# Optimization experiments

Hardware: AMD Instinct MI355X
Metric: run time of the kernel (lower is better)

The kernel has to match this reference:

```python
import jax, jax.numpy as jnp
import numpy as np

B, S, E = 4, 2048, 1024

def setup_inputs() -> dict:
    key = jax.random.key(0)
    ks = jax.random.split(key, 7)
    s = 1.0 / np.sqrt(E)
    return {
        "x":  jax.random.normal(ks[0], (B, S, E), jnp.float32),
        "Wq": jax.random.normal(ks[1], (E, E), jnp.float32) * s,
        "bq": jax.random.normal(ks[2], (E,), jnp.float32) * s,
        "Wk": jax.random.normal(ks[3], (E, E), jnp.float32) * s,
        "bk": jax.random.normal(ks[4], (E,), jnp.float32) * s,
        "Wv": jax.random.normal(ks[5], (E, E), jnp.float32) * s,
        "bv": jax.random.normal(ks[6], (E,), jnp.float32) * s,
    }

def reference(x, Wq, bq, Wk, bk, Wv, bv):
    # Linear layers: y = x @ W^T + b (torch nn.Linear convention)
    q = jnp.einsum('bse,fe->bsf', x, Wq) + bq
    k = jnp.einsum('bse,fe->bsf', x, Wk) + bk
    v = jnp.einsum('bse,fe->bsf', x, Wv) + bv
    inv_scale = jnp.asarray(E ** 0.5, x.dtype)
    scores = jnp.einsum('bqe,bke->bqk', q, k) / inv_scale  # [B,S,S]
    attn = jax.nn.softmax(scores, axis=-1)
    # dropout is identity in eval mode (deterministic reference)
    out = jnp.einsum('bqk,bke->bqe', attn, v)
    return out
```

## Files before the change

kernel.cpp:

```cpp
#include <hip/hip_runtime.h>
#include <hip/hip_bf16.h>
#include <cstdint>


typedef __attribute__((ext_vector_type(8))) short bf16x8;
typedef __attribute__((ext_vector_type(4))) float f32x4;

__device__ __forceinline__ unsigned short f2bf(float f) {
  union { float f; uint32_t u; } x; x.f = f;
  uint32_t u = x.u;
  return (unsigned short)((u + 0x7fffu + ((u >> 16) & 1u)) >> 16);
}

__device__ __forceinline__ void async_copy16(const void* g, void* l) {
  __builtin_amdgcn_global_load_lds(
      (const __attribute__((address_space(1))) void*)g,
      (__attribute__((address_space(3))) void*)l, 16, 0, 0);
}

__global__ __launch_bounds__(256) void convert_all(
    const float* __restrict__ x, const float* __restrict__ Wq,
    const float* __restrict__ Wk, const float* __restrict__ Wv,
    unsigned short* __restrict__ xb, unsigned short* __restrict__ Wb,
    float* __restrict__ rowsum) {
  const long X4 = (long)8192 * 1024 / 4;
  const long W4 = (long)1024 * 1024 / 4;
  if (blockIdx.x == gridDim.x - 1) {
    float4* r = (float4*)rowsum;
#pragma unroll
    for (int t = 0; t < 8; ++t)
      r[threadIdx.x + t * 256] = float4{0.f, 0.f, 0.f, 0.f};
    return;
  }
  long i = (long)blockIdx.x * 256 + threadIdx.x;
  const float* src; unsigned short* dst; long off;
  if (i < X4)             { src = x;  dst = xb;                    off = i; }
  else if (i < X4 + W4)   { src = Wq; dst = Wb;                    off = i - X4; }
  else if (i < X4 + 2*W4) { src = Wk; dst = Wb + (long)1024*1024;  off = i - X4 - W4; }
  else                    { src = Wv; dst = Wb + (long)2048*1024;  off = i - X4 - 2*W4; }
  const float4 v = ((const float4*)src)[off];
  ushort4 o;
  o.x = f2bf(v.x); o.y = f2bf(v.y); o.z = f2bf(v.z); o.w = f2bf(v.w);
  ((ushort4*)dst)[off] = o;
}

template <int MODE>
__global__ __launch_bounds__(256, 4) void gemm_bt(
    const unsigned short* __restrict__ Ab, const unsigned short* __restrict__ Bb,
    unsigned short* __restrict__ Cb, float* __restrict__ Cf,
    unsigned short* __restrict__ VT,
    const float* __restrict__ bias0, const float* __restrict__ bias1,
    const float* __restrict__ bias2, float* __restrict__ rowsum,
    int K, int N, float scale, long sA, long sB, long sC) {
  __shared__ unsigned short As[128 * 64];
  __shared__ unsigned short Bs[128 * 64];

  const int z = blockIdx.z;
  const unsigned short* A  = Ab + (long)z * sA;
  const unsigned short* Bm = Bb + (long)z * sB;

  const int tid  = threadIdx.x;
  const int lane = tid & 63;
  const int wave = tid >> 6;
  const int l15  = lane & 15;
  const int quad = lane >> 4;
  const int wm = (wave >> 1) * 64;
  const int wn = (wave & 1) * 64;

  const int bxd  = gridDim.x;
  const int flat = blockIdx.y * bxd + blockIdx.x;
  const int st = flat >> 6;
  const int inside = flat & 63;
  const int nstx = bxd >> 3;
  const int stx = st % nstx;
  const int sty = st / nstx;
  const int tile_m = (stx * 8 + (inside & 7)) * 128;
  const int tile_n = (sty * 8 + (inside >> 3)) * 128;

  const int rs8 = lane >> 3;
  const int kc  = (lane & 7) ^ rs8;
  const long lK = (long)K;
  const unsigned short* gA0 = A  + (long)(tile_m + wave * 32 + rs8) * lK + kc * 8;
  const unsigned short* gB0 = Bm + (long)(tile_n + wave * 32 + rs8) * lK + kc * 8;
  unsigned short* lA = &As[(wave * 32) * 64];
  unsigned short* lB = &Bs[(wave * 32) * 64];

  const int g0 = (0 * 4 + quad) ^ (l15 & 7);
  const int g1 = (1 * 4 + quad) ^ (l15 & 7);

  f32x4 acc[4][4] = {};

  for (int k0 = 0; k0 < K; k0 += 64) {
    __syncthreads();
#pragma unroll
    for (int t = 0; t < 4; ++t) {
      async_copy16(gA0 + (long)t * 8 * lK + k0, lA + t * 8 * 64);
      async_copy16(gB0 + (long)t * 8 * lK + k0, lB + t * 8 * 64);
    }
    __syncthreads();

#pragma unroll
    for (int s = 0; s < 2; ++s) {
      const int gs = s ? g1 : g0;
      bf16x8 af[4], bfr[4];
#pragma unroll
      for (int i = 0; i < 4; ++i)
        af[i] = *(const bf16x8*)&As[(wm + i * 16 + l15) * 64 + gs * 8];
#pragma unroll
      for (int j = 0; j < 4; ++j)
        bfr[j] = *(const bf16x8*)&Bs[(wn + j * 16 + l15) * 64 + gs * 8];
#pragma unroll
      for (int i = 0; i < 4; ++i)
#pragma unroll
        for (int j = 0; j < 4; ++j)
          acc[i][j] = __builtin_amdgcn_mfma_f32_16x16x32_bf16(af[i], bfr[j], acc[i][j], 0, 0, 0);
    }
  }

  if (MODE == 0) {
    const float* bias = (z == 0) ? bias0 : (z == 1) ? bias1 : bias2;
    if (z == 2) {
#pragma unroll
      for (int j = 0; j < 4; ++j) {
        const int col = tile_n + wn + j * 16 + l15;
        const float bv = bias[col];
#pragma unroll
        for (int i = 0; i < 4; ++i) {
          const int row0 = tile_m + wm + i * 16 + quad * 4;
          const int b = row0 >> 11;
          const int sx = row0 & 2047;
          ushort4 o;
          o.x = f2bf(acc[i][j][0] + bv);
          o.y = f2bf(acc[i][j][1] + bv);
          o.z = f2bf(acc[i][j][2] + bv);
          o.w = f2bf(acc[i][j][3] + bv);
          *(ushort4*)&VT[(long)b * 1024 * 2048 + (long)col * 2048 + sx] = o;
        }
      }
    } else {
      unsigned short* Cbz = Cb + (long)z * sC;
#pragma unroll
      for (int j = 0; j < 4; ++j) {
        const int col = tile_n + wn + j * 16 + l15;
        const float bv = bias[col];
#pragma unroll
        for (int i = 0; i < 4; ++i) {
          const int row0 = tile_m + wm + i * 16 + quad * 4;
#pragma unroll
          for (int r = 0; r < 4; ++r)
            Cbz[(long)(row0 + r) * N + col] = f2bf(acc[i][j][r] + bv);
        }
      }
    }
  } else if (MODE == 1) {
    unsigned short* Cbz = Cb + (long)z * sC;
    float part[16];
#pragma unroll
    for (int t = 0; t < 16; ++t) part[t] = 0.0f;
#pragma unroll
    for (int j = 0; j < 4; ++j) {
      const int col = tile_n + wn + j * 16 + l15;
#pragma unroll
      for (int i = 0; i < 4; ++i) {
        const int row0 = tile_m + wm + i * 16 + quad * 4;
#pragma unroll
        for (int r = 0; r < 4; ++r) {
          const float e = __expf(acc[i][j][r] * scale);
          part[i * 4 + r] += e;
          Cbz[(long)(row0 + r) * N + col] = f2bf(e);
        }
      }
    }
#pragma unroll
    for (int t = 0; t < 16; ++t)
#pragma unroll
      for (int o = 1; o < 16; o <<= 1)
        part[t] += __shfl_xor(part[t], o);
    if (l15 == 0) {
#pragma unroll
      for (int i = 0; i < 4; ++i) {
        const int row0 = tile_m + wm + i * 16 + quad * 4;
#pragma unroll
        for (int r = 0; r < 4; ++r)
          atomicAdd(&rowsum[z * 2048 + row0 + r], part[i * 4 + r]);
      }
    }
  } else {
    float* Cfz = Cf + (long)z * sC;
    float inv[16];
#pragma unroll
    for (int i = 0; i < 4; ++i) {
      const int row0 = tile_m + wm + i * 16 + quad * 4;
#pragma unroll
      for (int r = 0; r < 4; ++r)
        inv[i * 4 + r] = 1.0f / rowsum[z * 2048 + row0 + r];
    }
#pragma unroll
    for (int j = 0; j < 4; ++j) {
      const int col = tile_n + wn + j * 16 + l15;
#pragma unroll
      for (int i = 0; i < 4; ++i) {
        const int row0 = tile_m + wm + i * 16 + quad * 4;
#pragma unroll
        for (int r = 0; r < 4; ++r)
          Cfz[(long)(row0 + r) * N + col] = acc[i][j][r] * inv[i * 4 + r];
      }
    }
  }
}

extern "C" void kernel_launch(void* const* d_in, const int* in_sizes, int n_in,
                              void* d_out, int out_size, void* d_ws, size_t ws_size,
                              hipStream_t stream) {
  const float* x  = (const float*)d_in[0];
  const float* Wq = (const float*)d_in[1];
  const float* bq = (const float*)d_in[2];
  const float* Wk = (const float*)d_in[3];
  const float* bk = (const float*)d_in[4];
  const float* Wv = (const float*)d_in[5];
  const float* bv = (const float*)d_in[6];
  float* out = (float*)d_out;

  constexpr int Bt = 4, S = 2048, E = 1024;
  constexpr int M = Bt * S;

  unsigned short* xb = (unsigned short*)d_ws;
  unsigned short* Wb = xb + (size_t)M * E;
  unsigned short* Q  = Wb + (size_t)3 * E * E;
  unsigned short* Kb = Q + (size_t)M * E;
  unsigned short* VT = Kb + (size_t)M * E;
  unsigned short* P  = VT + (size_t)M * E;
  float* rowsum = (float*)(P + (size_t)Bt * S * S);

  const int conv_blocks = (M * E / 4 + 3 * (E * E / 4)) / 256 + 1;
  convert_all<<<dim3(conv_blocks), dim3(256), 0, stream>>>(x, Wq, Wk, Wv, xb, Wb, rowsum);

  gemm_bt<0><<<dim3(M / 128, E / 128, 3), dim3(256), 0, stream>>>(
      xb, Wb, Q, nullptr, VT, bq, bk, bv, nullptr, E, E, 1.0f,
      0L, (long)E * E, (long)M * E);

  gemm_bt<1><<<dim3(S / 128, S / 128, Bt), dim3(256), 0, stream>>>(
      Q, Kb, P, nullptr, nullptr, nullptr, nullptr, nullptr, rowsum,
      E, S, 1.0f / 32.0f, (long)S * E, (long)S * E, (long)S * S);

  gemm_bt<2><<<dim3(S / 128, E / 128, Bt), dim3(256), 0, stream>>>(
      P, VT, nullptr, out, nullptr, nullptr, nullptr, nullptr, rowsum,
      S, E, 1.0f, (long)S * S, (long)E * S, (long)S * E);
}
```

Measured before the change: 236.0 us.

## Double-buffer GEMM LDS with 8-wave larger tiles and XCD-aware block remap

The GEMM kernel moves to 512-thread workgroups with templated larger tiles (up to 256x256) and two LDS buffers. The next K-tile is prefetched with async global-to-LDS loads while the current one is consumed, using explicit vmcnt waits and barriers plus s_setprio around the MFMA bursts. Block indices are remapped across the 8 XCDs instead of using the old 8x8 supertile swizzle. This aims to hide load latency and raise arithmetic intensity, at the cost of more LDS and registers per block and lower occupancy.

```diff
diff --git a/kernel.cpp b/kernel.cpp
--- a/kernel.cpp
+++ b/kernel.cpp
@@ -1,5 +1,4 @@
 #include <hip/hip_runtime.h>
-#include <hip/hip_bf16.h>
 #include <cstdint>
 
 
@@ -16,6 +15,21 @@
   __builtin_amdgcn_global_load_lds(
       (const __attribute__((address_space(1))) void*)g,
       (__attribute__((address_space(3))) void*)l, 16, 0, 0);
+}
+
+#define FENCE() asm volatile("" ::: "memory")
+
+__device__ __forceinline__ void wg_bar() {
+  FENCE();
+  __builtin_amdgcn_s_barrier();
+  FENCE();
+}
+
+template <int N>
+__device__ __forceinline__ void vm_wait() {
+  if constexpr (N == 0)      asm volatile("s_waitcnt vmcnt(0)" ::: "memory");
+  else if constexpr (N == 6) asm volatile("s_waitcnt vmcnt(6)" ::: "memory");
+  else                       asm volatile("s_waitcnt vmcnt(8)" ::: "memory");
 }
 
 __global__ __launch_bounds__(256) void convert_all(
@@ -44,18 +58,38 @@
   ((ushort4*)dst)[off] = o;
 }
 
-template <int MODE>
-__global__ __launch_bounds__(256, 4) void gemm_bt(
+template <int MODE, int BM, int BN, int WM, int WN>
+__global__ __launch_bounds__(512, 2) void gemm_bt(
     const unsigned short* __restrict__ Ab, const unsigned short* __restrict__ Bb,
     unsigned short* __restrict__ Cb, float* __restrict__ Cf,
     unsigned short* __restrict__ VT,
     const float* __restrict__ bias0, const float* __restrict__ bias1,
     const float* __restrict__ bias2, float* __restrict__ rowsum,
     int K, int N, float scale, long sA, long sB, long sC) {
-  __shared__ unsigned short As[128 * 64];
-  __shared__ unsigned short Bs[128 * 64];
-
-  const int z = blockIdx.z;
+  static_assert(WM * WN == 8, "8 waves");
+  static_assert(BN / WN == 64, "per-wave col span must be 64");
+  constexpr int M_rep = BM / WM / 16;
+  constexpr int N_rep = 4;
+  constexpr int PH    = M_rep / 2;
+  constexpr int LA    = BM / 64;
+  constexpr int LB    = BN / 64;
+  constexpr int LOADS = LA + LB;
+
+  __shared__ unsigned short As[2][BM * 64];
+  __shared__ unsigned short Bs[2][BN * 64];
+
+  const int gx = gridDim.x, gy = gridDim.y;
+  const int nwg = gx * gy * (int)gridDim.z;
+  int flat = ((int)blockIdx.z * gy + (int)blockIdx.y) * gx + (int)blockIdx.x;
+  flat = (flat & 7) * (nwg >> 3) + (flat >> 3);
+  const int bx = flat % gx;
+  const int r2 = flat / gx;
+  const int by = r2 % gy;
+  const int z  = r2 / gy;
+
+  const int tile_m = bx * BM;
+  const int tile_n = by * BN;
+
   const unsigned short* A  = Ab + (long)z * sA;
   const unsigned short* Bm = Bb + (long)z * sB;
 
@@ -64,69 +98,94 @@
   const int wave = tid >> 6;
   const int l15  = lane & 15;
   const int quad = lane >> 4;
-  const int wm = (wave >> 1) * 64;
-  const int wn = (wave & 1) * 64;
-
-  const int bxd  = gridDim.x;
-  const int flat = blockIdx.y * bxd + blockIdx.x;
-  const int st = flat >> 6;
-  const int inside = flat & 63;
-  const int nstx = bxd >> 3;
-  const int stx = st % nstx;
-  const int sty = st / nstx;
-  const int tile_m = (stx * 8 + (inside & 7)) * 128;
-  const int tile_n = (sty * 8 + (inside >> 3)) * 128;
+  const int wn   = wave % WN;
+  const int wm   = wave / WN;
+  const int wmr  = wm * (BM / WM);
+  const int wnc  = wn * 64;
 
   const int rs8 = lane >> 3;
   const int kc  = (lane & 7) ^ rs8;
   const long lK = (long)K;
-  const unsigned short* gA0 = A  + (long)(tile_m + wave * 32 + rs8) * lK + kc * 8;
-  const unsigned short* gB0 = Bm + (long)(tile_n + wave * 32 + rs8) * lK + kc * 8;
-  unsigned short* lA = &As[(wave * 32) * 64];
-  unsigned short* lB = &Bs[(wave * 32) * 64];
-
-  const int g0 = (0 * 4 + quad) ^ (l15 & 7);
-  const int g1 = (1 * 4 + quad) ^ (l15 & 7);
-
-  f32x4 acc[4][4] = {};
-
-  for (int k0 = 0; k0 < K; k0 += 64) {
-    __syncthreads();
-#pragma unroll
-    for (int t = 0; t < 4; ++t) {
-      async_copy16(gA0 + (long)t * 8 * lK + k0, lA + t * 8 * 64);
-      async_copy16(gB0 + (long)t * 8 * lK + k0, lB + t * 8 * 64);
-    }
-    __syncthreads();
-
-#pragma unroll
-    for (int s = 0; s < 2; ++s) {
-      const int gs = s ? g1 : g0;
-      bf16x8 af[4], bfr[4];
-#pragma unroll
-      for (int i = 0; i < 4; ++i)
-        af[i] = *(const bf16x8*)&As[(wm + i * 16 + l15) * 64 + gs * 8];
-#pragma unroll
-      for (int j = 0; j < 4; ++j)
-        bfr[j] = *(const bf16x8*)&Bs[(wn + j * 16 + l15) * 64 + gs * 8];
-#pragma unroll
-      for (int i = 0; i < 4; ++i)
-#pragma unroll
-        for (int j = 0; j < 4; ++j)
-          acc[i][j] = __builtin_amdgcn_mfma_f32_16x16x32_bf16(af[i], bfr[j], acc[i][j], 0, 0, 0);
-    }
+  const unsigned short* gA0 = A  + (long)(tile_m + wave * (BM / 8) + rs8) * lK + kc * 8;
+  const unsigned short* gB0 = Bm + (long)(tile_n + wave * (BN / 8) + rs8) * lK + kc * 8;
+
+  auto stage = [&](int k0, int pb) {
+    unsigned short* la = &As[pb][(wave * (BM / 8)) * 64];
+    unsigned short* lb = &Bs[pb][(wave * (BN / 8)) * 64];
+#pragma unroll
+    for (int t = 0; t < LA; ++t)
+      async_copy16(gA0 + (long)(t * 8) * lK + k0, la + t * 8 * 64);
+#pragma unroll
+    for (int t = 0; t < LB; ++t)
+      async_copy16(gB0 + (long)(t * 8) * lK + k0, lb + t * 8 * 64);
+  };
+
+  const int NT = K >> 6;
+  f32x4 acc[M_rep][N_rep] = {};
+
+  stage(0, 0);
+  stage(64, 1);
+  vm_wait<LOADS>();
+  wg_bar();
+
+  int p = 0;
+  for (int t = 0; t < NT; ++t) {
+    const unsigned short* as = &As[p][0];
+    const unsigned short* bs = &Bs[p][0];
+    bf16x8 bfr[N_rep][2];
+#pragma unroll
+    for (int ph = 0; ph < PH; ++ph) {
+      bf16x8 af[2][2];
+#pragma unroll
+      for (int ii = 0; ii < 2; ++ii) {
+        const int row = wmr + (ph * 2 + ii) * 16 + l15;
+#pragma unroll
+        for (int kk = 0; kk < 2; ++kk)
+          af[ii][kk] = *(const bf16x8*)&as[row * 64 + (((kk * 4 + quad) ^ (l15 & 7)) << 3)];
+      }
+      if (ph == 0) {
+#pragma unroll
+        for (int j = 0; j < N_rep; ++j) {
+          const int row = wnc + j * 16 + l15;
+#pragma unroll
+          for (int kk = 0; kk < 2; ++kk)
+            bfr[j][kk] = *(const bf16x8*)&bs[row * 64 + (((kk * 4 + quad) ^ (l15 & 7)) << 3)];
+        }
+      }
+      wg_bar();
+      __builtin_amdgcn_s_setprio(1);
+#pragma unroll
+      for (int ii = 0; ii < 2; ++ii)
+#pragma unroll
+        for (int j = 0; j < N_rep; ++j)
+#pragma unroll
+          for (int kk = 0; kk < 2; ++kk)
+            acc[ph * 2 + ii][j] = __builtin_amdgcn_mfma_f32_16x16x32_bf16(
+                af[ii][kk], bfr[j][kk], acc[ph * 2 + ii][j], 0, 0, 0);
+      __builtin_amdgcn_s_setprio(0);
+      wg_bar();
+    }
+    if (t + 2 < NT) {
+      stage((t + 2) << 6, p);
+      vm_wait<LOADS>();
+      wg_bar();
+    } else if (t + 1 < NT) {
+      vm_wait<0>();
+      wg_bar();
+    }
+    p ^= 1;
   }
 
-  if (MODE == 0) {
+  if constexpr (MODE == 0) {
     const float* bias = (z == 0) ? bias0 : (z == 1) ? bias1 : bias2;
     if (z == 2) {
 #pragma unroll
-      for (int j = 0; j < 4; ++j) {
-        const int col = tile_n + wn + j * 16 + l15;
+      for (int j = 0; j < N_rep; ++j) {
+        const int col = tile_n + wnc + j * 16 + l15;
         const float bv = bias[col];
 #pragma unroll
-        for (int i = 0; i < 4; ++i) {
-          const int row0 = tile_m + wm + i * 16 + quad * 4;
+        for (int i = 0; i < M_rep; ++i) {
+          const int row0 = tile_m + wmr + i * 16 + quad * 4;
           const int b = row0 >> 11;
           const int sx = row0 & 2047;
           ushort4 o;
@@ -140,29 +199,29 @@
     } else {
       unsigned short* Cbz = Cb + (long)z * sC;
 #pragma unroll
-      for (int j = 0; j < 4; ++j) {
-        const int col = tile_n + wn + j * 16 + l15;
+      for (int j = 0; j < N_rep; ++j) {
+        const int col = tile_n + wnc + j * 16 + l15;
         const float bv = bias[col];
 #pragma unroll
-        for (int i = 0; i < 4; ++i) {
-          const int row0 = tile_m + wm + i * 16 + quad * 4;
+        for (int i = 0; i < M_rep; ++i) {
+          const int row0 = tile_m + wmr + i * 16 + quad * 4;
 #pragma unroll
           for (int r = 0; r < 4; ++r)
             Cbz[(long)(row0 + r) * N + col] = f2bf(acc[i][j][r] + bv);
         }
       }
     }
-  } else if (MODE == 1) {
+  } else if constexpr (MODE == 1) {
     unsigned short* Cbz = Cb + (long)z * sC;
-    float part[16];
-#pragma unroll
-    for (int t = 0; t < 16; ++t) part[t] = 0.0f;
-#pragma unroll
-    for (int j = 0; j < 4; ++j) {
-      const int col = tile_n + wn + j * 16 + l15;
-#pragma unroll
-      for (int i = 0; i < 4; ++i) {
-        const int row0 = tile_m + wm + i * 16 + quad * 4;
+    float part[M_rep * 4];
+#pragma unroll
+    for (int t = 0; t < M_rep * 4; ++t) part[t] = 0.0f;
+#pragma unroll
+    for (int j = 0; j < N_rep; ++j) {
+      const int col = tile_n + wnc + j * 16 + l15;
+#pragma unroll
+      for (int i = 0; i < M_rep; ++i) {
+        const int row0 = tile_m + wmr + i * 16 + quad * 4;
 #pragma unroll
         for (int r = 0; r < 4; ++r) {
           const float e = __expf(acc[i][j][r] * scale);
@@ -172,14 +231,14 @@
       }
     }
 #pragma unroll
-    for (int t = 0; t < 16; ++t)
+    for (int t = 0; t < M_rep * 4; ++t)
 #pragma unroll
       for (int o = 1; o < 16; o <<= 1)
         part[t] += __shfl_xor(part[t], o);
     if (l15 == 0) {
 #pragma unroll
-      for (int i = 0; i < 4; ++i) {
-        const int row0 = tile_m + wm + i * 16 + quad * 4;
+      for (int i = 0; i < M_rep; ++i) {
+        const int row0 = tile_m + wmr + i * 16 + quad * 4;
 #pragma unroll
         for (int r = 0; r < 4; ++r)
           atomicAdd(&rowsum[z * 2048 + row0 + r], part[i * 4 + r]);
@@ -187,20 +246,20 @@
     }
   } else {
     float* Cfz = Cf + (long)z * sC;
-    float inv[16];
-#pragma unroll
-    for (int i = 0; i < 4; ++i) {
-      const int row0 = tile_m + wm + i * 16 + quad * 4;
+    float inv[M_rep * 4];
+#pragma unroll
+    for (int i = 0; i < M_rep; ++i) {
+      const int row0 = tile_m + wmr + i * 16 + quad * 4;
 #pragma unroll
       for (int r = 0; r < 4; ++r)
         inv[i * 4 + r] = 1.0f / rowsum[z * 2048 + row0 + r];
     }
 #pragma unroll
-    for (int j = 0; j < 4; ++j) {
-      const int col = tile_n + wn + j * 16 + l15;
-#pragma unroll
-      for (int i = 0; i < 4; ++i) {
-        const int row0 = tile_m + wm + i * 16 + quad * 4;
+    for (int j = 0; j < N_rep; ++j) {
+      const int col = tile_n + wnc + j * 16 + l15;
+#pragma unroll
+      for (int i = 0; i < M_rep; ++i) {
+        const int row0 = tile_m + wmr + i * 16 + quad * 4;
 #pragma unroll
         for (int r = 0; r < 4; ++r)
           Cfz[(long)(row0 + r) * N + col] = acc[i][j][r] * inv[i * 4 + r];
@@ -235,15 +294,15 @@
   const int conv_blocks = (M * E / 4 + 3 * (E * E / 4)) / 256 + 1;
   convert_all<<<dim3(conv_blocks), dim3(256), 0, stream>>>(x, Wq, Wk, Wv, xb, Wb, rowsum);
 
-  gemm_bt<0><<<dim3(M / 128, E / 128, 3), dim3(256), 0, stream>>>(
+  gemm_bt<0, 128, 256, 2, 4><<<dim3(M / 128, E / 256, 3), dim3(512), 0, stream>>>(
       xb, Wb, Q, nullptr, VT, bq, bk, bv, nullptr, E, E, 1.0f,
       0L, (long)E * E, (long)M * E);
 
-  gemm_bt<1><<<dim3(S / 128, S / 128, Bt), dim3(256), 0, stream>>>(
+  gemm_bt<1, 256, 256, 2, 4><<<dim3(S / 256, S / 256, Bt), dim3(512), 0, stream>>>(
       Q, Kb, P, nullptr, nullptr, nullptr, nullptr, nullptr, rowsum,
       E, S, 1.0f / 32.0f, (long)S * E, (long)S * E, (long)S * S);
 
-  gemm_bt<2><<<dim3(S / 128, E / 128, Bt), dim3(256), 0, stream>>>(
+  gemm_bt<2, 256, 128, 4, 2><<<dim3(S / 256, E / 128, Bt), dim3(512), 0, stream>>>(
       P, VT, nullptr, out, nullptr, nullptr, nullptr, nullptr, rowsum,
       S, E, 1.0f, (long)S * S, (long)E * S, (long)S * E);
 }
```

Result: slower. 291.2 us (+23.4%).

## Replace QK^T scores GEMM with 256x256 double-buffered 8-wave pipelined kernel

Applied to the files above, without the earlier changes.

Replaces the generic 128x128 gemm_bt MODE 1 launch for the Q·K^T scores with a dedicated kernel that uses 256x256 tiles, 512 threads and double-buffered LDS. Global-to-LDS async loads for later k-steps are interleaved with MFMA phases, using explicit vmcnt waits, raw barriers and s_setprio. The goal is to hide load latency and raise data reuse per tile, at the cost of much more LDS (128 KB per block) and register pressure, which lowers occupancy. The exp, bf16 store and atomic row-sum epilogue is kept.

```diff
diff --git a/kernel.cpp b/kernel.cpp
--- a/kernel.cpp
+++ b/kernel.cpp
@@ -1,5 +1,4 @@
 #include <hip/hip_runtime.h>
-#include <hip/hip_bf16.h>
 #include <cstdint>
 
 
@@ -16,6 +15,21 @@
   __builtin_amdgcn_global_load_lds(
       (const __attribute__((address_space(1))) void*)g,
       (__attribute__((address_space(3))) void*)l, 16, 0, 0);
+}
+
+#define FENCE() asm volatile("" ::: "memory")
+
+__device__ __forceinline__ void wg_bar() {
+  FENCE();
+  __builtin_amdgcn_s_barrier();
+  FENCE();
+}
+
+template <int N>
+__device__ __forceinline__ void vm_wait() {
+  if constexpr (N == 0)      asm volatile("s_waitcnt vmcnt(0)" ::: "memory");
+  else if constexpr (N == 4) asm volatile("s_waitcnt vmcnt(4)" ::: "memory");
+  else                       asm volatile("s_waitcnt vmcnt(8)" ::: "memory");
 }
 
 __global__ __launch_bounds__(256) void convert_all(
@@ -117,7 +131,7 @@
     }
   }
 
-  if (MODE == 0) {
+  if constexpr (MODE == 0) {
     const float* bias = (z == 0) ? bias0 : (z == 1) ? bias1 : bias2;
     if (z == 2) {
 #pragma unroll
@@ -152,39 +166,6 @@
         }
       }
     }
-  } else if (MODE == 1) {
-    unsigned short* Cbz = Cb + (long)z * sC;
-    float part[16];
-#pragma unroll
-    for (int t = 0; t < 16; ++t) part[t] = 0.0f;
-#pragma unroll
-    for (int j = 0; j < 4; ++j) {
-      const int col = tile_n + wn + j * 16 + l15;
-#pragma unroll
-      for (int i = 0; i < 4; ++i) {
-        const int row0 = tile_m + wm + i * 16 + quad * 4;
-#pragma unroll
-        for (int r = 0; r < 4; ++r) {
-          const float e = __expf(acc[i][j][r] * scale);
-          part[i * 4 + r] += e;
-          Cbz[(long)(row0 + r) * N + col] = f2bf(e);
-        }
-      }
-    }
-#pragma unroll
-    for (int t = 0; t < 16; ++t)
-#pragma unroll
-      for (int o = 1; o < 16; o <<= 1)
-        part[t] += __shfl_xor(part[t], o);
-    if (l15 == 0) {
-#pragma unroll
-      for (int i = 0; i < 4; ++i) {
-        const int row0 = tile_m + wm + i * 16 + quad * 4;
-#pragma unroll
-        for (int r = 0; r < 4; ++r)
-          atomicAdd(&rowsum[z * 2048 + row0 + r], part[i * 4 + r]);
-      }
-    }
   } else {
     float* Cfz = Cf + (long)z * sC;
     float inv[16];
@@ -205,6 +186,132 @@
         for (int r = 0; r < 4; ++r)
           Cfz[(long)(row0 + r) * N + col] = acc[i][j][r] * inv[i * 4 + r];
       }
+    }
+  }
+}
+
+__global__ __launch_bounds__(512, 2) void scores_8ph(
+    const unsigned short* __restrict__ Qb, const unsigned short* __restrict__ Kb,
+    unsigned short* __restrict__ P, float* __restrict__ rowsum) {
+  constexpr int NT = 16;
+  constexpr long SE = 2048L * 1024;
+  constexpr float SC = 1.0f / 32.0f;
+
+  __shared__ unsigned short As[2][2][128 * 64];
+  __shared__ unsigned short Bs[2][2][128 * 64];
+
+  const int z = blockIdx.z;
+  const unsigned short* A  = Qb + (long)z * SE;
+  const unsigned short* Bm = Kb + (long)z * SE;
+  const int tile_m = blockIdx.x * 256;
+  const int tile_n = blockIdx.y * 256;
+
+  const int tid  = threadIdx.x;
+  const int lane = tid & 63;
+  const int wave = tid >> 6;
+  const int l15  = lane & 15;
+  const int quad = lane >> 4;
+
+  const int rs8 = lane >> 3;
+  const int kc  = (lane & 7) ^ rs8;
+  const unsigned short* gA0 = A  + (long)(tile_m + wave * 16 + rs8) * 1024 + kc * 8;
+  const unsigned short* gB0 = Bm + (long)(tile_n + wave * 16 + rs8) * 1024 + kc * 8;
+
+  auto stA = [&](int T, int h) {
+    if (T < NT) {
+      const int pb = T & 1, k0 = T << 6;
+      async_copy16(gA0 + (long)(h * 128) * 1024 + k0,     &As[pb][h][(wave * 16) * 64]);
+      async_copy16(gA0 + (long)(h * 128 + 8) * 1024 + k0, &As[pb][h][(wave * 16 + 8) * 64]);
+    }
+  };
+  auto stB = [&](int T, int h) {
+    if (T < NT) {
+      const int pb = T & 1, k0 = T << 6;
+      async_copy16(gB0 + (long)(h * 128) * 1024 + k0,     &Bs[pb][h][(wave * 16) * 64]);
+      async_copy16(gB0 + (long)(h * 128 + 8) * 1024 + k0, &Bs[pb][h][(wave * 16 + 8) * 64]);
+    }
+  };
+
+  stA(0, 0); stB(0, 0); stB(0, 1); stA(0, 1);
+  stA(1, 0); stB(1, 0);
+  vm_wait<4>();
+  wg_bar();
+
+  f32x4 acc[16][2] = {};
+
+  for (int t = 0; t < NT; ++t) {
+    const int c = t & 1;
+    bf16x8 bfr[2][2];
+#pragma unroll
+    for (int p = 0; p < 4; ++p) {
+      if (p == 0)      stB(t + 1, 1);
+      else if (p == 1) stA(t + 1, 1);
+      else if (p == 2) stA(t + 2, 0);
+      else             stB(t + 2, 0);
+      bf16x8 af[4][2];
+#pragma unroll
+      for (int ii = 0; ii < 4; ++ii) {
+        const int f = p * 4 + ii;
+        const int rih = (f & 7) * 16 + l15;
+#pragma unroll
+        for (int kk = 0; kk < 2; ++kk)
+          af[ii][kk] = *(const bf16x8*)
+              &As[c][f >> 3][rih * 64 + (((kk * 4 + quad) ^ (l15 & 7)) << 3)];
+      }
+      if (p == 0) {
+#pragma unroll
+        for (int j = 0; j < 2; ++j) {
+          const int rih = (wave & 3) * 32 + j * 16 + l15;
+#pragma unroll
+          for (int kk = 0; kk < 2; ++kk)
+            bfr[j][kk] = *(const bf16x8*)
+                &Bs[c][wave >> 2][rih * 64 + (((kk * 4 + quad) ^ (l15 & 7)) << 3)];
+        }
+      }
+      wg_bar();
+      asm volatile("s_waitcnt lgkmcnt(0)" ::: "memory");
+      __builtin_amdgcn_s_setprio(1);
+#pragma unroll
+      for (int ii = 0; ii < 4; ++ii)
+#pragma unroll
+        for (int j = 0; j < 2; ++j)
+#pragma unroll
+          for (int kk = 0; kk < 2; ++kk)
+            acc[p * 4 + ii][j] = __builtin_amdgcn_mfma_f32_16x16x32_bf16(
+                af[ii][kk], bfr[j][kk], acc[p * 4 + ii][j], 0, 0, 0);
+      __builtin_amdgcn_s_setprio(0);
+      if (p == 3) {
+        if (t + 2 < NT)      vm_wait<4>();
+        else if (t + 1 < NT) vm_wait<0>();
+      }
+      wg_bar();
+    }
+  }
+
+  unsigned short* Pz = P + (long)z * (2048L * 2048);
+#pragma unroll
+  for (int f = 0; f < 16; ++f) {
+    float pr[4] = {0.f, 0.f, 0.f, 0.f};
+    const int row0 = tile_m + f * 16 + quad * 4;
+#pragma unroll
+    for (int j = 0; j < 2; ++j) {
+      const int col = tile_n + wave * 32 + j * 16 + l15;
+#pragma unroll
+      for (int r = 0; r < 4; ++r) {
+        const float e = __expf(acc[f][j][r] * SC);
+        pr[r] += e;
+        Pz[(long)(row0 + r) * 2048 + col] = f2bf(e);
+      }
+    }
+#pragma unroll
+    for (int r = 0; r < 4; ++r)
+#pragma unroll
+      for (int o = 1; o < 16; o <<= 1)
+        pr[r] += __shfl_xor(pr[r], o);
+    if (l15 == 0) {
+#pragma unroll
+      for (int r = 0; r < 4; ++r)
+        atomicAdd(&rowsum[z * 2048 + row0 + r], pr[r]);
     }
   }
 }
@@ -239,9 +346,8 @@
       xb, Wb, Q, nullptr, VT, bq, bk, bv, nullptr, E, E, 1.0f,
       0L, (long)E * E, (long)M * E);
 
-  gemm_bt<1><<<dim3(S / 128, S / 128, Bt), dim3(256), 0, stream>>>(
-      Q, Kb, P, nullptr, nullptr, nullptr, nullptr, nullptr, rowsum,
-      E, S, 1.0f / 32.0f, (long)S * E, (long)S * E, (long)S * S);
+  scores_8ph<<<dim3(S / 256, S / 256, Bt), dim3(512), 0, stream>>>(
+      Q, Kb, P, rowsum);
 
   gemm_bt<2><<<dim3(S / 128, E / 128, Bt), dim3(256), 0, stream>>>(
       P, VT, nullptr, out, nullptr, nullptr, nullptr, nullptr, rowsum,
```

Result: slower. 263.1 us (+11.5%).

## Double-buffer LDS tiles with async prefetch in attention GEMMs

Applied to the files above, without the earlier changes.

Adds a double-buffered shared-memory variant of the GEMM kernel. While the current K-tile is being computed, the next tile is fetched with global_load_lds, ordered by explicit vmcnt waits and raw barriers. The aim is to hide global-load latency behind MFMA work in the QK^T and PV GEMMs. The projection GEMM keeps the single-buffer path. LDS use doubles to 64KB per block, which may limit occupancy from the requested 4 blocks per CU.

```diff
diff --git a/kernel.cpp b/kernel.cpp
--- a/kernel.cpp
+++ b/kernel.cpp
@@ -1,5 +1,4 @@
 #include <hip/hip_runtime.h>
-#include <hip/hip_bf16.h>
 #include <cstdint>
 
 
@@ -16,6 +15,21 @@
   __builtin_amdgcn_global_load_lds(
       (const __attribute__((address_space(1))) void*)g,
       (__attribute__((address_space(3))) void*)l, 16, 0, 0);
+}
+
+#define FENCE() asm volatile("" ::: "memory")
+
+__device__ __forceinline__ void wg_bar() {
+  FENCE();
+  __builtin_amdgcn_s_barrier();
+  FENCE();
+}
+
+template <int N>
+__device__ __forceinline__ void vm_wait() {
+  if constexpr (N == 0)      asm volatile("s_waitcnt vmcnt(0)" ::: "memory");
+  else if constexpr (N == 8) asm volatile("s_waitcnt vmcnt(8)" ::: "memory");
+  else                       asm volatile("s_waitcnt vmcnt(4)" ::: "memory");
 }
 
 __global__ __launch_bounds__(256) void convert_all(
@@ -44,7 +58,7 @@
   ((ushort4*)dst)[off] = o;
 }
 
-template <int MODE>
+template <int MODE, int DBUF>
 __global__ __launch_bounds__(256, 4) void gemm_bt(
     const unsigned short* __restrict__ Ab, const unsigned short* __restrict__ Bb,
     unsigned short* __restrict__ Cb, float* __restrict__ Cf,
@@ -52,8 +66,9 @@
     const float* __restrict__ bias0, const float* __restrict__ bias1,
     const float* __restrict__ bias2, float* __restrict__ rowsum,
     int K, int N, float scale, long sA, long sB, long sC) {
-  __shared__ unsigned short As[128 * 64];
-  __shared__ unsigned short Bs[128 * 64];
+  constexpr int NBUF = DBUF ? 2 : 1;
+  __shared__ unsigned short As[NBUF][128 * 64];
+  __shared__ unsigned short Bs[NBUF][128 * 64];
 
   const int z = blockIdx.z;
   const unsigned short* A  = Ab + (long)z * sA;
@@ -82,42 +97,68 @@
   const long lK = (long)K;
   const unsigned short* gA0 = A  + (long)(tile_m + wave * 32 + rs8) * lK + kc * 8;
   const unsigned short* gB0 = Bm + (long)(tile_n + wave * 32 + rs8) * lK + kc * 8;
-  unsigned short* lA = &As[(wave * 32) * 64];
-  unsigned short* lB = &Bs[(wave * 32) * 64];
 
   const int g0 = (0 * 4 + quad) ^ (l15 & 7);
   const int g1 = (1 * 4 + quad) ^ (l15 & 7);
 
   f32x4 acc[4][4] = {};
 
-  for (int k0 = 0; k0 < K; k0 += 64) {
-    __syncthreads();
+  auto stage = [&](int k0, int pb) {
 #pragma unroll
     for (int t = 0; t < 4; ++t) {
-      async_copy16(gA0 + (long)t * 8 * lK + k0, lA + t * 8 * 64);
-      async_copy16(gB0 + (long)t * 8 * lK + k0, lB + t * 8 * 64);
-    }
-    __syncthreads();
-
+      async_copy16(gA0 + (long)t * 8 * lK + k0, &As[pb][(wave * 32 + t * 8) * 64]);
+      async_copy16(gB0 + (long)t * 8 * lK + k0, &Bs[pb][(wave * 32 + t * 8) * 64]);
+    }
+  };
+
+  auto compute = [&](int pb) {
 #pragma unroll
     for (int s = 0; s < 2; ++s) {
       const int gs = s ? g1 : g0;
       bf16x8 af[4], bfr[4];
 #pragma unroll
       for (int i = 0; i < 4; ++i)
-        af[i] = *(const bf16x8*)&As[(wm + i * 16 + l15) * 64 + gs * 8];
+        af[i] = *(const bf16x8*)&As[pb][(wm + i * 16 + l15) * 64 + gs * 8];
 #pragma unroll
       for (int j = 0; j < 4; ++j)
-        bfr[j] = *(const bf16x8*)&Bs[(wn + j * 16 + l15) * 64 + gs * 8];
+        bfr[j] = *(const bf16x8*)&Bs[pb][(wn + j * 16 + l15) * 64 + gs * 8];
 #pragma unroll
       for (int i = 0; i < 4; ++i)
 #pragma unroll
         for (int j = 0; j < 4; ++j)
           acc[i][j] = __builtin_amdgcn_mfma_f32_16x16x32_bf16(af[i], bfr[j], acc[i][j], 0, 0, 0);
     }
+  };
+
+  if constexpr (DBUF == 0) {
+    for (int k0 = 0; k0 < K; k0 += 64) {
+      __syncthreads();
+      stage(k0, 0);
+      __syncthreads();
+      compute(0);
+    }
+  } else {
+    const int NT = K >> 6;
+    stage(0, 0);
+    stage(64, 1);
+    vm_wait<8>();
+    wg_bar();
+    for (int t = 0; t < NT; ++t) {
+      const int p = t & 1;
+      compute(p);
+      wg_bar();
+      if (t + 2 < NT) {
+        stage((t + 2) << 6, p);
+        vm_wait<8>();
+        wg_bar();
+      } else if (t + 1 < NT) {
+        vm_wait<0>();
+        wg_bar();
+      }
+    }
   }
 
-  if (MODE == 0) {
+  if constexpr (MODE == 0) {
     const float* bias = (z == 0) ? bias0 : (z == 1) ? bias1 : bias2;
     if (z == 2) {
 #pragma unroll
@@ -152,7 +193,7 @@
         }
       }
     }
-  } else if (MODE == 1) {
+  } else if constexpr (MODE == 1) {
     unsigned short* Cbz = Cb + (long)z * sC;
     float part[16];
 #pragma unroll
@@ -235,15 +276,15 @@
   const int conv_blocks = (M * E / 4 + 3 * (E * E / 4)) / 256 + 1;
   convert_all<<<dim3(conv_blocks), dim3(256), 0, stream>>>(x, Wq, Wk, Wv, xb, Wb, rowsum);
 
-  gemm_bt<0><<<dim3(M / 128, E / 128, 3), dim3(256), 0, stream>>>(
+  gemm_bt<0, 0><<<dim3(M / 128, E / 128, 3), dim3(256), 0, stream>>>(
       xb, Wb, Q, nullptr, VT, bq, bk, bv, nullptr, E, E, 1.0f,
       0L, (long)E * E, (long)M * E);
 
-  gemm_bt<1><<<dim3(S / 128, S / 128, Bt), dim3(256), 0, stream>>>(
+  gemm_bt<1, 1><<<dim3(S / 128, S / 128, Bt), dim3(256), 0, stream>>>(
       Q, Kb, P, nullptr, nullptr, nullptr, nullptr, nullptr, rowsum,
       E, S, 1.0f / 32.0f, (long)S * E, (long)S * E, (long)S * S);
 
-  gemm_bt<2><<<dim3(S / 128, E / 128, Bt), dim3(256), 0, stream>>>(
+  gemm_bt<2, 1><<<dim3(S / 128, E / 128, Bt), dim3(256), 0, stream>>>(
       P, VT, nullptr, out, nullptr, nullptr, nullptr, nullptr, rowsum,
       S, E, 1.0f, (long)S * S, (long)E * S, (long)S * E);
 }
```

After: 253.7 us. +7.5%, slower.
